# Performance work log

Measured on AMD Instinct MI355X. Metric: run time of the kernel, lower is better.

Reference implementation:

```python
import jax, jax.numpy as jnp
import numpy as np

NUM_LAYERS = 24
LN_EPS = 1e-5


def setup_inputs() -> dict:
    key = jax.random.key(0)
    ks = jax.random.split(key, 8)
    B, S = 256, 8192
    x = jax.random.uniform(ks[0], (B, S, 5), dtype=jnp.float32)
    # per-layer LayerNorm(4) params (torch default init: weight=1, bias=0; use
    # randomized values so the gather is non-trivial)
    ln_w = 1.0 + 0.1 * jax.random.normal(ks[1], (NUM_LAYERS, 4), dtype=jnp.float32)
    ln_b = 0.1 * jax.random.normal(ks[2], (NUM_LAYERS, 4), dtype=jnp.float32)
    # MLP 5 -> 64 -> 32 -> 1 (dropout inactive in eval mode)
    W1 = jax.random.normal(ks[3], (64, 5), dtype=jnp.float32) / np.sqrt(5)
    b1 = jnp.zeros((64,), dtype=jnp.float32)
    W2 = jax.random.normal(ks[4], (32, 64), dtype=jnp.float32) / np.sqrt(64)
    b2 = jnp.zeros((32,), dtype=jnp.float32)
    W3 = jax.random.normal(ks[5], (1, 32), dtype=jnp.float32) / np.sqrt(32)
    b3 = jnp.zeros((1,), dtype=jnp.float32)
    return {"x": x, "ln_w": ln_w, "ln_b": ln_b, "W1": W1, "b1": b1,
            "W2": W2, "b2": b2, "W3": W3, "b3": b3}


def reference(x, ln_w, ln_b, W1, b1, W2, b2, W3, b3):
    B, S, _ = x.shape
    x_flat = x.reshape(-1, 5)                      # [N, 5]
    layer_pos = x_flat[:, -1]                      # [N]
    layer_ids = jnp.clip((layer_pos * NUM_LAYERS).astype(jnp.int32), 0, NUM_LAYERS - 1)
    feats = x_flat[:, :4]                          # [N, 4]
    # vectorized per-token LayerNorm: gather per-token gamma/beta by layer id
    mean = jnp.mean(feats, axis=-1, keepdims=True)
    var = jnp.mean(jnp.square(feats - mean), axis=-1, keepdims=True)  # biased, as torch LN
    normed = (feats - mean) * jax.lax.rsqrt(var + LN_EPS)
    normed = normed * ln_w[layer_ids] + ln_b[layer_ids]               # [N, 4]
    x_norm = jnp.concatenate([normed, layer_pos[:, None]], axis=1)    # [N, 5]
    h = jax.nn.relu(x_norm @ W1.T + b1)            # [N, 64]
    h = jax.nn.relu(h @ W2.T + b2)                 # [N, 32]
    scores = h @ W3.T + b3                         # [N, 1]
    return scores.reshape(B, S)
```

## Files before the change

kernel.cpp:

```cpp
#include <hip/hip_runtime.h>
#include <stdint.h>

#define NUM_LAYERS 24
#define LN_EPS 1e-5f
#define N_ROWS (256 * 8192)
#define NUM_BLOCKS 2048

typedef __attribute__((ext_vector_type(4)))  uint32_t u32x4;
typedef __attribute__((ext_vector_type(16))) float    f32x16;
typedef __attribute__((ext_vector_type(2)))  float    f32x2;
typedef __attribute__((ext_vector_type(2)))  __fp16   h16x2;

__device__ __forceinline__ uint32_t pk_f16_rtz(float lo, float hi) {
    h16x2 v = __builtin_amdgcn_cvt_pkrtz(lo, hi);
    uint32_t u; __builtin_memcpy(&u, &v, 4);
    return u;
}
__device__ __forceinline__ uint32_t pk_f16_rne(float lo, float hi) {
    __fp16 a = (__fp16)lo, b = (__fp16)hi;
    uint16_t ua, ub;
    __builtin_memcpy(&ua, &a, 2); __builtin_memcpy(&ub, &b, 2);
    return (uint32_t)ua | ((uint32_t)ub << 16);
}
__device__ __forceinline__ uint32_t pk_relu_f16(uint32_t d) {
    h16x2 v; __builtin_memcpy(&v, &d, 4);
    h16x2 z = {(__fp16)0.0f, (__fp16)0.0f};
    v = __builtin_elementwise_max(v, z);
    uint32_t u; __builtin_memcpy(&u, &v, 4);
    return u;
}

__device__ __forceinline__ u32x4 make_frag(uint32_t d0, uint32_t d1,
                                           uint32_t d2, uint32_t d3) {
    u32x4 f; f.x = d0; f.y = d1; f.z = d2; f.w = d3;
    return f;
}

__device__ __forceinline__ void mfma_l1(f32x16& d0, f32x16& d1,
                                        const u32x4& a0, const u32x4& a1,
                                        const u32x4& b) {
    asm("s_nop 2\n\t"
        "v_mfma_f32_32x32x16_f16 %0, %2, %4, 0\n\t"
        "v_mfma_f32_32x32x16_f16 %1, %3, %4, 0"
        : "=&v"(d0), "=&v"(d1)
        : "v"(a0), "v"(a1), "v"(b));
}
__device__ __forceinline__ void mfma_l2z(f32x16& c0, f32x16& c1,
                                         const u32x4& w0, const u32x4& w1,
                                         const u32x4& w2, const u32x4& w3,
                                         const u32x4& h00, const u32x4& h01,
                                         const u32x4& h02, const u32x4& h03,
                                         const u32x4& h10, const u32x4& h11,
                                         const u32x4& h12, const u32x4& h13) {
    asm("s_nop 2\n\t"
        "v_mfma_f32_32x32x16_f16 %0, %2, %6, 0\n\t"
        "v_mfma_f32_32x32x16_f16 %1, %2, %10, 0\n\t"
        "v_mfma_f32_32x32x16_f16 %0, %3, %7, %0\n\t"
        "v_mfma_f32_32x32x16_f16 %1, %3, %11, %1\n\t"
        "v_mfma_f32_32x32x16_f16 %0, %4, %8, %0\n\t"
        "v_mfma_f32_32x32x16_f16 %1, %4, %12, %1\n\t"
        "v_mfma_f32_32x32x16_f16 %0, %5, %9, %0\n\t"
        "v_mfma_f32_32x32x16_f16 %1, %5, %13, %1"
        : "=&v"(c0), "=&v"(c1)
        : "v"(w0), "v"(w1), "v"(w2), "v"(w3),
          "v"(h00), "v"(h01), "v"(h02), "v"(h03),
          "v"(h10), "v"(h11), "v"(h12), "v"(h13));
}
__device__ __forceinline__ void mfma_fence2(f32x16& c0, f32x16& c1) {
    asm volatile("s_nop 7\n\ts_nop 7\n\ts_nop 7" : "+v"(c0), "+v"(c1));
}

__device__ __forceinline__ int sigma_k(int p) {
    int hh = (p >> 2) & 1;
    int base = (p & 31) - 4 * hh;
    int r = (base & 3) + 4 * (base >> 3);
    return 32 * (p >> 5) + 16 * (r >> 3) + 8 * hh + (r & 7);
}

__global__ __launch_bounds__(256, 4) void router_mfma(
    const float* __restrict__ x,
    const float* __restrict__ ln_w,
    const float* __restrict__ ln_b,
    const float* __restrict__ W1,
    const float* __restrict__ b1,
    const float* __restrict__ W2,
    const float* __restrict__ b2,
    const float* __restrict__ W3,
    const float* __restrict__ b3,
    float* __restrict__ out)
{
    __shared__ uint32_t s_a1[2 * 64 * 4];
    __shared__ uint32_t s_w2[4 * 64 * 4];
    __shared__ float    s_wb[8 * 64 * 4];
    __shared__ float    s_ln[8 * NUM_LAYERS];

    const int t = threadIdx.x;

    if (t < 8 * NUM_LAYERS) {
        const int q = t & 7, lid = t >> 3;
        s_ln[q * NUM_LAYERS + lid] =
            (q < 4) ? ln_w[lid * 4 + q] : ln_b[lid * 4 + (q - 4)];
    }
    if (t < 128) {
        const int mt = t >> 6, ln = t & 63;
        const int n32l = ln & 31, hl = ln >> 5;
        uint32_t d0 = 0, d1 = 0, d2 = 0;
        if (!hl) {
            const int k = sigma_k(mt * 32 + n32l);
            d0 = pk_f16_rne(W1[k * 5 + 0], W1[k * 5 + 1]);
            d1 = pk_f16_rne(W1[k * 5 + 2], W1[k * 5 + 3]);
            d2 = pk_f16_rne(W1[k * 5 + 4], b1[k]);
        }
        uint32_t* p = &s_a1[(mt * 64 + ln) * 4];
        p[0] = d0; p[1] = d1; p[2] = d2; p[3] = 0;
    }
    {
        const int kt = t >> 6, ln = t & 63;
        const int n32l = ln & 31, hl = ln >> 5;
        const float* wp = W2 + n32l * 64 + kt * 16 + hl * 8;
        const float4 lo = *(const float4*)(wp);
        const float4 hi = *(const float4*)(wp + 4);
        uint32_t* p = &s_w2[(kt * 64 + ln) * 4];
        p[0] = pk_f16_rne(lo.x, lo.y);
        p[1] = pk_f16_rne(lo.z, lo.w);
        p[2] = pk_f16_rne(hi.x, hi.y);
        p[3] = pk_f16_rne(hi.z, hi.w);
    }
#pragma unroll
    for (int e = t; e < 512; e += 256) {
        const int r2 = e >> 6, ln = e & 63;
        const int hl = ln >> 5;
        const int n = ((2 * r2) & 3) + 8 * (r2 >> 1) + 4 * hl;
        float* p = &s_wb[e * 4];
        p[0] = W3[n]; p[1] = W3[n + 1];
        p[2] = b2[n]; p[3] = b2[n + 1];
    }
    __syncthreads();

    const int lane = t & 63;
    const int wid  = t >> 6;
    const int h    = lane >> 5;

    u32x4 a1f[2], w2f[4];
#pragma unroll
    for (int mt = 0; mt < 2; ++mt)
        a1f[mt] = *(const u32x4*)&s_a1[(mt * 64 + lane) * 4];
#pragma unroll
    for (int kt = 0; kt < 4; ++kt)
        w2f[kt] = *(const u32x4*)&s_w2[(kt * 64 + lane) * 4];

    const float b3v = b3[0];
    const f32x2 z2 = {0.0f, 0.0f};

    const int w = blockIdx.x * 4 + wid;
    const size_t rowBase = (size_t)w * 256;

    float4 cv[4];
    float  cl[4];
#pragma unroll
    for (int g = 0; g < 4; ++g) {
        const float* p = x + (rowBase + 64 * g + lane) * 5;
        cv[g] = *(const float4*)p;
        cl[g] = p[4];
    }

#pragma unroll
    for (int g = 0; g < 4; ++g) {
        const size_t gbase = rowBase + 64 * g;

        int lid = (int)(cl[g] * (float)NUM_LAYERS);
        lid = lid < 0 ? 0 : (lid > NUM_LAYERS - 1 ? NUM_LAYERS - 1 : lid);

        const float m  = (cv[g].x + cv[g].y + cv[g].z + cv[g].w) * 0.25f;
        const float d0 = cv[g].x - m, d1 = cv[g].y - m,
                    d2 = cv[g].z - m, d3 = cv[g].w - m;
        const float var = (d0 * d0 + d1 * d1 + d2 * d2 + d3 * d3) * 0.25f;
        const float r   = rsqrtf(var + LN_EPS);

        const float xn0 = fmaf(d0, r * s_ln[0 * 24 + lid], s_ln[4 * 24 + lid]);
        const float xn1 = fmaf(d1, r * s_ln[1 * 24 + lid], s_ln[5 * 24 + lid]);
        const float xn2 = fmaf(d2, r * s_ln[2 * 24 + lid], s_ln[6 * 24 + lid]);
        const float xn3 = fmaf(d3, r * s_ln[3 * 24 + lid], s_ln[7 * 24 + lid]);

        const uint32_t e0 = pk_f16_rtz(xn0, xn1);
        const uint32_t e1 = pk_f16_rtz(xn2, xn3);
        const uint32_t e2 = pk_f16_rtz(cl[g], 1.0f);
        const uint32_t x0 = __shfl_xor((int)e0, 32, 64);
        const uint32_t x1 = __shfl_xor((int)e1, 32, 64);
        const uint32_t x2 = __shfl_xor((int)e2, 32, 64);

        const u32x4 bf_t0 = make_frag(e0, e1, e2, 0u);
        const u32x4 bf_t1 = make_frag(x0, x1, x2, 0u);

        u32x4 h1f0[4], h1f1[4];
        {
            f32x16 c1a, c1b;
            mfma_l1(c1a, c1b, a1f[0], a1f[1], bf_t0);
            mfma_fence2(c1a, c1b);
#pragma unroll
            for (int kt = 0; kt < 4; ++kt) {
                const f32x16& c1 = (kt < 2) ? c1a : c1b;
                const int roff = 8 * (kt & 1);
                uint32_t dw[4];
#pragma unroll
                for (int d = 0; d < 4; ++d)
                    dw[d] = pk_relu_f16(
                        pk_f16_rtz(c1[roff + 2 * d], c1[roff + 2 * d + 1]));
                h1f0[kt] = make_frag(dw[0], dw[1], dw[2], dw[3]);
            }
        }
        {
            f32x16 c1a, c1b;
            mfma_l1(c1a, c1b, a1f[0], a1f[1], bf_t1);
            mfma_fence2(c1a, c1b);
#pragma unroll
            for (int kt = 0; kt < 4; ++kt) {
                const f32x16& c1 = (kt < 2) ? c1a : c1b;
                const int roff = 8 * (kt & 1);
                uint32_t dw[4];
#pragma unroll
                for (int d = 0; d < 4; ++d)
                    dw[d] = pk_relu_f16(
                        pk_f16_rtz(c1[roff + 2 * d], c1[roff + 2 * d + 1]));
                h1f1[kt] = make_frag(dw[0], dw[1], dw[2], dw[3]);
            }
        }

        f32x16 c2_0, c2_1;
        mfma_l2z(c2_0, c2_1,
                 w2f[0], w2f[1], w2f[2], w2f[3],
                 h1f0[0], h1f0[1], h1f0[2], h1f0[3],
                 h1f1[0], h1f1[1], h1f1[2], h1f1[3]);
        mfma_fence2(c2_0, c2_1);

        f32x2 acc0 = z2, acc1 = z2;
#pragma unroll
        for (int r2 = 0; r2 < 8; ++r2) {
            const float4 wb = *(const float4*)&s_wb[(r2 * 64 + lane) * 4];
            f32x2 v0 = {c2_0[2 * r2] + wb.z, c2_0[2 * r2 + 1] + wb.w};
            f32x2 v1 = {c2_1[2 * r2] + wb.z, c2_1[2 * r2 + 1] + wb.w};
            v0 = __builtin_elementwise_max(v0, z2);
            v1 = __builtin_elementwise_max(v1, z2);
            const f32x2 w3v = {wb.x, wb.y};
            acc0 = v0 * w3v + acc0;
            acc1 = v1 * w3v + acc1;
        }
        float q0 = acc0.x + acc0.y;
        float q1 = acc1.x + acc1.y;
        q0 += __shfl_xor(q0, 32, 64);
        q1 += __shfl_xor(q1, 32, 64);

        out[gbase + lane] = (h ? q1 : q0) + b3v;
    }
}

extern "C" void kernel_launch(void* const* d_in, const int* in_sizes, int n_in,
                              void* d_out, int out_size, void* d_ws, size_t ws_size,
                              hipStream_t stream) {
    const float* x    = (const float*)d_in[0];
    const float* ln_w = (const float*)d_in[1];
    const float* ln_b = (const float*)d_in[2];
    const float* W1   = (const float*)d_in[3];
    const float* b1   = (const float*)d_in[4];
    const float* W2   = (const float*)d_in[5];
    const float* b2   = (const float*)d_in[6];
    const float* W3   = (const float*)d_in[7];
    const float* b3   = (const float*)d_in[8];
    float* out = (float*)d_out;

    router_mfma<<<NUM_BLOCKS, 256, 0, stream>>>(x, ln_w, ln_b, W1, b1, W2, b2,
                                                W3, b3, out);
}
```

Before: 104.6 us.

## Move layer-3 dot product onto MFMA and fold b2 into layer-2 accumulator init

The layer-2 MFMA chain now starts from a preloaded b2 accumulator instead of zero, so the separate bias add goes away. The scalar per-lane W3 dot product and cross-half shuffle reduction are replaced by a ReLU/fp16 repack of the layer-2 outputs and four extra MFMAs against a W3 fragment that is nonzero only in one row. Launch bounds drop from 4 to 3 blocks per CU to leave room for the larger register footprint. The trade is extra MFMA work, mostly wasted on zero rows, plus fp16 rounding of layer-2 activations and lower occupancy, in exchange for removing VALU FMA and shuffle work.

```diff
diff --git a/kernel.cpp b/kernel.cpp
--- a/kernel.cpp
+++ b/kernel.cpp
@@ -45,26 +45,38 @@
         : "=&v"(d0), "=&v"(d1)
         : "v"(a0), "v"(a1), "v"(b));
 }
-__device__ __forceinline__ void mfma_l2z(f32x16& c0, f32x16& c1,
-                                         const u32x4& w0, const u32x4& w1,
-                                         const u32x4& w2, const u32x4& w3,
-                                         const u32x4& h00, const u32x4& h01,
-                                         const u32x4& h02, const u32x4& h03,
-                                         const u32x4& h10, const u32x4& h11,
-                                         const u32x4& h12, const u32x4& h13) {
+__device__ __forceinline__ void mfma_l2(f32x16& c0, f32x16& c1, const f32x16& cinit,
+                                        const u32x4& w0, const u32x4& w1,
+                                        const u32x4& w2, const u32x4& w3,
+                                        const u32x4& h00, const u32x4& h01,
+                                        const u32x4& h02, const u32x4& h03,
+                                        const u32x4& h10, const u32x4& h11,
+                                        const u32x4& h12, const u32x4& h13) {
     asm("s_nop 2\n\t"
-        "v_mfma_f32_32x32x16_f16 %0, %2, %6, 0\n\t"
-        "v_mfma_f32_32x32x16_f16 %1, %2, %10, 0\n\t"
-        "v_mfma_f32_32x32x16_f16 %0, %3, %7, %0\n\t"
-        "v_mfma_f32_32x32x16_f16 %1, %3, %11, %1\n\t"
+        "v_mfma_f32_32x32x16_f16 %0, %3, %7, %2\n\t"
+        "v_mfma_f32_32x32x16_f16 %1, %3, %11, %2\n\t"
         "v_mfma_f32_32x32x16_f16 %0, %4, %8, %0\n\t"
         "v_mfma_f32_32x32x16_f16 %1, %4, %12, %1\n\t"
         "v_mfma_f32_32x32x16_f16 %0, %5, %9, %0\n\t"
-        "v_mfma_f32_32x32x16_f16 %1, %5, %13, %1"
+        "v_mfma_f32_32x32x16_f16 %1, %5, %13, %1\n\t"
+        "v_mfma_f32_32x32x16_f16 %0, %6, %10, %0\n\t"
+        "v_mfma_f32_32x32x16_f16 %1, %6, %14, %1"
         : "=&v"(c0), "=&v"(c1)
-        : "v"(w0), "v"(w1), "v"(w2), "v"(w3),
+        : "v"(cinit), "v"(w0), "v"(w1), "v"(w2), "v"(w3),
           "v"(h00), "v"(h01), "v"(h02), "v"(h03),
           "v"(h10), "v"(h11), "v"(h12), "v"(h13));
+}
+__device__ __forceinline__ void mfma_l3(f32x16& s0, f32x16& s1,
+                                        const u32x4& a30, const u32x4& a31,
+                                        const u32x4& b00, const u32x4& b01,
+                                        const u32x4& b10, const u32x4& b11) {
+    asm("s_nop 2\n\t"
+        "v_mfma_f32_32x32x16_f16 %0, %2, %4, 0\n\t"
+        "v_mfma_f32_32x32x16_f16 %1, %2, %6, 0\n\t"
+        "v_mfma_f32_32x32x16_f16 %0, %3, %5, %0\n\t"
+        "v_mfma_f32_32x32x16_f16 %1, %3, %7, %1"
+        : "=&v"(s0), "=&v"(s1)
+        : "v"(a30), "v"(a31), "v"(b00), "v"(b01), "v"(b10), "v"(b11));
 }
 __device__ __forceinline__ void mfma_fence2(f32x16& c0, f32x16& c1) {
     asm volatile("s_nop 7\n\ts_nop 7\n\ts_nop 7" : "+v"(c0), "+v"(c1));
@@ -77,7 +89,7 @@
     return 32 * (p >> 5) + 16 * (r >> 3) + 8 * hh + (r & 7);
 }
 
-__global__ __launch_bounds__(256, 4) void router_mfma(
+__global__ __launch_bounds__(256, 3) void router_mfma(
     const float* __restrict__ x,
     const float* __restrict__ ln_w,
     const float* __restrict__ ln_b,
@@ -91,7 +103,7 @@
 {
     __shared__ uint32_t s_a1[2 * 64 * 4];
     __shared__ uint32_t s_w2[4 * 64 * 4];
-    __shared__ float    s_wb[8 * 64 * 4];
+    __shared__ float    s_b2[8 * 64 * 2];
     __shared__ float    s_ln[8 * NUM_LAYERS];
 
     const int t = threadIdx.x;
@@ -131,14 +143,14 @@
         const int r2 = e >> 6, ln = e & 63;
         const int hl = ln >> 5;
         const int n = ((2 * r2) & 3) + 8 * (r2 >> 1) + 4 * hl;
-        float* p = &s_wb[e * 4];
-        p[0] = W3[n]; p[1] = W3[n + 1];
-        p[2] = b2[n]; p[3] = b2[n + 1];
+        s_b2[e * 2 + 0] = b2[n];
+        s_b2[e * 2 + 1] = b2[n + 1];
     }
     __syncthreads();
 
     const int lane = t & 63;
     const int wid  = t >> 6;
+    const int n32  = lane & 31;
     const int h    = lane >> 5;
 
     u32x4 a1f[2], w2f[4];
@@ -149,8 +161,30 @@
     for (int kt = 0; kt < 4; ++kt)
         w2f[kt] = *(const u32x4*)&s_w2[(kt * 64 + lane) * 4];
 
+    f32x16 c2init;
+#pragma unroll
+    for (int r2 = 0; r2 < 8; ++r2) {
+        const f32x2 bp = *(const f32x2*)&s_b2[(r2 * 64 + lane) * 2];
+        c2init[2 * r2]     = bp.x;
+        c2init[2 * r2 + 1] = bp.y;
+    }
+
+    u32x4 a3f[2] = {make_frag(0, 0, 0, 0), make_frag(0, 0, 0, 0)};
+    if (n32 == 0) {
+#pragma unroll
+        for (int kt = 0; kt < 2; ++kt) {
+            uint32_t dw[4];
+#pragma unroll
+            for (int d = 0; d < 4; ++d) {
+                const int j0 = 2 * d, j1 = 2 * d + 1;
+                const int u0 = (j0 & 3) + 16 * kt + 8 * (j0 >> 2) + 4 * h;
+                const int u1 = (j1 & 3) + 16 * kt + 8 * (j1 >> 2) + 4 * h;
+                dw[d] = pk_f16_rne(W3[u0], W3[u1]);
+            }
+            a3f[kt] = make_frag(dw[0], dw[1], dw[2], dw[3]);
+        }
+    }
     const float b3v = b3[0];
-    const f32x2 z2 = {0.0f, 0.0f};
 
     const int w = blockIdx.x * 4 + wid;
     const size_t rowBase = (size_t)w * 256;
@@ -227,30 +261,34 @@
         }
 
         f32x16 c2_0, c2_1;
-        mfma_l2z(c2_0, c2_1,
-                 w2f[0], w2f[1], w2f[2], w2f[3],
-                 h1f0[0], h1f0[1], h1f0[2], h1f0[3],
-                 h1f1[0], h1f1[1], h1f1[2], h1f1[3]);
+        mfma_l2(c2_0, c2_1, c2init,
+                w2f[0], w2f[1], w2f[2], w2f[3],
+                h1f0[0], h1f0[1], h1f0[2], h1f0[3],
+                h1f1[0], h1f1[1], h1f1[2], h1f1[3]);
         mfma_fence2(c2_0, c2_1);
 
-        f32x2 acc0 = z2, acc1 = z2;
-#pragma unroll
-        for (int r2 = 0; r2 < 8; ++r2) {
-            const float4 wb = *(const float4*)&s_wb[(r2 * 64 + lane) * 4];
-            f32x2 v0 = {c2_0[2 * r2] + wb.z, c2_0[2 * r2 + 1] + wb.w};
-            f32x2 v1 = {c2_1[2 * r2] + wb.z, c2_1[2 * r2 + 1] + wb.w};
-            v0 = __builtin_elementwise_max(v0, z2);
-            v1 = __builtin_elementwise_max(v1, z2);
-            const f32x2 w3v = {wb.x, wb.y};
-            acc0 = v0 * w3v + acc0;
-            acc1 = v1 * w3v + acc1;
-        }
-        float q0 = acc0.x + acc0.y;
-        float q1 = acc1.x + acc1.y;
-        q0 += __shfl_xor(q0, 32, 64);
-        q1 += __shfl_xor(q1, 32, 64);
-
-        out[gbase + lane] = (h ? q1 : q0) + b3v;
+        u32x4 sb0[2], sb1[2];
+#pragma unroll
+        for (int kt = 0; kt < 2; ++kt) {
+            uint32_t dwa[4], dwb[4];
+#pragma unroll
+            for (int d = 0; d < 4; ++d) {
+                const int rr = 8 * kt + 2 * d;
+                dwa[d] = pk_relu_f16(pk_f16_rtz(c2_0[rr], c2_0[rr + 1]));
+                dwb[d] = pk_relu_f16(pk_f16_rtz(c2_1[rr], c2_1[rr + 1]));
+            }
+            sb0[kt] = make_frag(dwa[0], dwa[1], dwa[2], dwa[3]);
+            sb1[kt] = make_frag(dwb[0], dwb[1], dwb[2], dwb[3]);
+        }
+
+        f32x16 s0, s1;
+        mfma_l3(s0, s1, a3f[0], a3f[1], sb0[0], sb0[1], sb1[0], sb1[1]);
+        mfma_fence2(s0, s1);
+
+        if (!h) {
+            out[gbase + n32]      = s0[0] + b3v;
+            out[gbase + 32 + n32] = s1[0] + b3v;
+        }
     }
 }
 
```

New measurement: 106.6 us. About the same (+1.9%).
